# Kernel optimization log

Measured on AMD Instinct MI355X. Metric: run time of the kernel, lower is better.

Reference implementation:

```python
import jax, jax.numpy as jnp
import numpy as np
from jax import lax

B, C, D, H, W = 4, 384, 16, 16, 16
DSTATE, DCONV, EXPAND = 16, 4, 2
DIN = C * EXPAND            # 768
DTRANK = (C + 15) // 16     # 24
EPS = 1e-5


def setup_inputs() -> dict:
    ks = jax.random.split(jax.random.key(0), 12)
    g = lambda k, shape, s=0.02: jax.random.normal(k, shape, jnp.float32) * s
    return {
        "x": jax.random.normal(ks[0], (B, C, D, H, W), jnp.float32),
        "gsc_w1": g(ks[1], (C, C, 3, 3, 3)), "gsc_b1": jnp.zeros((C,), jnp.float32),
        "gsc_w2": g(ks[2], (C, C, 3, 3, 3)), "gsc_b2": jnp.zeros((C,), jnp.float32),
        "gsc_w3": g(ks[3], (C, C, 1, 1, 1)), "gsc_b3": jnp.zeros((C,), jnp.float32),
        "gsc_w4": g(ks[4], (C, C, 1, 1, 1)), "gsc_b4": jnp.zeros((C,), jnp.float32),
        "ln_g": jnp.ones((C,), jnp.float32), "ln_b": jnp.zeros((C,), jnp.float32),
        "in_proj_w": g(ks[5], (2 * DIN, C)),
        "conv1d_w": g(ks[6], (DIN, 1, DCONV), 0.1), "conv1d_b": jnp.zeros((DIN,), jnp.float32),
        "x_proj_w": g(ks[7], (DTRANK + 2 * DSTATE, DIN)),
        "dt_proj_w": g(ks[8], (DIN, DTRANK), 0.1), "dt_proj_b": jnp.full((DIN,), -4.0, jnp.float32),
        "A_log": jnp.log(jnp.tile(jnp.arange(1, DSTATE + 1, dtype=jnp.float32), (DIN, 1))),
        "D_skip": jnp.ones((DIN,), jnp.float32),
        "out_proj_w": g(ks[9], (C, DIN)),
    }


def _conv3d(x, w, b, pad):
    y = lax.conv_general_dilated(x, w, (1, 1, 1), [(pad, pad)] * 3,
                                 dimension_numbers=("NCDHW", "OIDHW", "NCDHW"))
    return y + b[None, :, None, None, None]


def _inorm(x):  # InstanceNorm3d, affine=False, biased variance
    m = x.mean((2, 3, 4), keepdims=True)
    v = x.var((2, 3, 4), keepdims=True)
    return (x - m) * lax.rsqrt(v + EPS)


def _forward(x, gsc_w1, gsc_b1, gsc_w2, gsc_b2, gsc_w3, gsc_b3, gsc_w4, gsc_b4,
             ln_g, ln_b, in_proj_w, conv1d_w, conv1d_b, x_proj_w,
             dt_proj_w, dt_proj_b, A_log, D_skip, out_proj_w):
    relu = jax.nn.relu
    # ---- GSC block (residual gated spatial conv) ----
    x1 = relu(_inorm(_conv3d(x, gsc_w1, gsc_b1, 1)))
    x1 = relu(_inorm(_conv3d(x1, gsc_w2, gsc_b2, 1)))
    x2 = relu(_inorm(_conv3d(x, gsc_w3, gsc_b3, 0)))
    xg = relu(_inorm(_conv3d(x1 + x2, gsc_w4, gsc_b4, 0))) + x
    # ---- MambaLayer: flatten voxels to tokens ----
    Bn = xg.shape[0]
    L = D * H * W
    t = xg.reshape(Bn, C, L).swapaxes(1, 2)                     # [B, L, C]
    mu = t.mean(-1, keepdims=True)
    var = t.var(-1, keepdims=True)
    tn = (t - mu) * lax.rsqrt(var + EPS) * ln_g + ln_b          # LayerNorm
    # ---- Mamba block ----
    xz = tn @ in_proj_w.T                                       # [B, L, 2*DIN]
    xin, z = jnp.split(xz, 2, axis=-1)
    xc = xin.swapaxes(1, 2)                                     # [B, DIN, L]
    xc = lax.conv_general_dilated(xc, conv1d_w, (1,), [(DCONV - 1, 0)],
                                  dimension_numbers=("NCH", "OIH", "NCH"),
                                  feature_group_count=DIN)      # causal depthwise conv
    u = jax.nn.silu(xc + conv1d_b[None, :, None]).swapaxes(1, 2)  # [B, L, DIN]
    dbl = u @ x_proj_w.T                                        # [B, L, DTRANK+2N]
    dt, Bm, Cm = jnp.split(dbl, [DTRANK, DTRANK + DSTATE], axis=-1)
    dt = jax.nn.softplus(dt @ dt_proj_w.T + dt_proj_b)          # [B, L, DIN]
    A = -jnp.exp(A_log)                                         # [DIN, N]

    def step(h, inp):  # h: [B, DIN, N]
        dt_t, B_t, C_t, u_t = inp
        dA = jnp.exp(dt_t[:, :, None] * A)
        h = dA * h + (dt_t * u_t)[:, :, None] * B_t[:, None, :]
        return h, jnp.einsum("bdn,bn->bd", h, C_t)

    h0 = jnp.zeros((Bn, DIN, DSTATE), x.dtype)
    _, ys = lax.scan(step, h0, (dt.swapaxes(0, 1), Bm.swapaxes(0, 1),
                                Cm.swapaxes(0, 1), u.swapaxes(0, 1)))
    y = ys.swapaxes(0, 1) + u * D_skip                          # [B, L, DIN]
    y = y * jax.nn.silu(z)
    out = y @ out_proj_w.T                                      # [B, L, C]
    return out.swapaxes(1, 2).reshape(Bn, C, D, H, W)


def reference(x, gsc_w1, gsc_b1, gsc_w2, gsc_b2, gsc_w3, gsc_b3, gsc_w4, gsc_b4,
              ln_g, ln_b, in_proj_w, conv1d_w, conv1d_b, x_proj_w,
              dt_proj_w, dt_proj_b, A_log, D_skip, out_proj_w):
    return _forward(x, gsc_w1, gsc_b1, gsc_w2, gsc_b2, gsc_w3, gsc_b3, gsc_w4, gsc_b4,
                    ln_g, ln_b, in_proj_w, conv1d_w, conv1d_b, x_proj_w,
                    dt_proj_w, dt_proj_b, A_log, D_skip, out_proj_w)
```

## Files before the change

### kernel.cpp

```cpp
#include <hip/hip_runtime.h>
#include <math.h>

#define CDIM 384
#define SDIM 4096
#define BDIM 4
#define DINC 768
#define NST  16
#define NCHUNK 64
#define LCHUNK 64
#define PSTRIDE 6291456

typedef unsigned short ushort_t;
typedef unsigned int uint_t;
typedef __attribute__((ext_vector_type(4))) float f32x4;
typedef __attribute__((ext_vector_type(8))) short bf16x8;

__device__ __forceinline__ ushort_t f2bf(float f) {
    union { float f; uint_t u; } v; v.f = f;
    uint_t r = v.u + 0x7FFFu + ((v.u >> 16) & 1u);
    return (ushort_t)(r >> 16);
}
__device__ __forceinline__ float bf2f(ushort_t u) {
    union { uint_t i; float f; } v; v.i = ((uint_t)u) << 16; return v.f;
}
__device__ __forceinline__ uint_t pk2(float a, float b) {
    return (uint_t)f2bf(a) | ((uint_t)f2bf(b) << 16);
}
__device__ __forceinline__ void gl16(const ushort_t* g, ushort_t* l) {
    __builtin_amdgcn_global_load_lds(
        (const __attribute__((address_space(1))) void*)(g),
        (__attribute__((address_space(3))) void*)(l), 16, 0, 0);
}

__device__ __forceinline__ void wconv_body(const float* __restrict__ W,
                                           ushort_t* __restrict__ Wb, int idx) {
    const float* wp = W + (size_t)idx * 27;
#pragma unroll
    for (int tap = 0; tap < 27; ++tap)
        Wb[(size_t)tap * (CDIM * CDIM) + idx] = f2bf(wp[tap]);
}
__device__ __forceinline__ void cvt_body(const float* __restrict__ src,
                                         ushort_t* __restrict__ dst, int i) {
    float4 v = ((const float4*)src)[i];
    uint2 o; o.x = pk2(v.x, v.y); o.y = pk2(v.z, v.w);
    ((uint2*)dst)[i] = o;
}
__global__ __launch_bounds__(256)
void prep_weights_kernel(const float* w1, const float* w2, const float* w3,
                         const float* w4, const float* ipw, const float* opw,
                         const float* xpw,
                         ushort_t* Wb1, ushort_t* Wb2, ushort_t* w3b, ushort_t* w4b,
                         ushort_t* ipwb, ushort_t* opwb, ushort_t* xpwb) {
    const int bid = blockIdx.x, t = threadIdx.x;
    if      (bid < 576)  wconv_body(w1, Wb1, bid * 256 + t);
    else if (bid < 1152) wconv_body(w2, Wb2, (bid - 576) * 256 + t);
    else if (bid < 1296) cvt_body(w3, w3b, (bid - 1152) * 256 + t);
    else if (bid < 1440) cvt_body(w4, w4b, (bid - 1296) * 256 + t);
    else if (bid < 2016) cvt_body(ipw, ipwb, (bid - 1440) * 256 + t);
    else if (bid < 2304) cvt_body(opw, opwb, (bid - 2016) * 256 + t);
    else                 cvt_body(xpw, xpwb, (bid - 2304) * 256 + t);
}

__global__ __launch_bounds__(384)
void pad_kernel(const float* __restrict__ src, ushort_t* __restrict__ Xp) {
    const int blk = blockIdx.x;
    const int b = blk >> 8, d = (blk >> 4) & 15, h = blk & 15;
    const int ci = threadIdx.x;
    const float* sp = src + (size_t)(b * CDIM + ci) * SDIM + d * 256 + h * 16;
    ushort_t* dp = Xp + ((((size_t)(b * 18 + d + 1) * 18) + (h + 1)) * 18 + 1) * CDIM + ci;
#pragma unroll
    for (int w = 0; w < 16; ++w)
        dp[(size_t)w * CDIM] = f2bf(sp[w]);
}

__global__ __launch_bounds__(384)
void pad_fuse2_kernel(const ushort_t* __restrict__ P0, const ushort_t* __restrict__ P1,
                      const float* __restrict__ stats, ushort_t* __restrict__ Xp) {
    const int blk = blockIdx.x;
    const int b = blk >> 8, d = (blk >> 4) & 15, h = blk & 15;
    const int ci = threadIdx.x;
    const size_t o = (size_t)(b * CDIM + ci) * SDIM + d * 256 + h * 16;
    const float m = stats[(b * CDIM + ci) * 2], r = stats[(b * CDIM + ci) * 2 + 1];
    union { uint4 q[2]; ushort_t u[16]; } a, c;
    a.q[0] = ((const uint4*)(P0 + o))[0]; a.q[1] = ((const uint4*)(P0 + o))[1];
    c.q[0] = ((const uint4*)(P1 + o))[0]; c.q[1] = ((const uint4*)(P1 + o))[1];
    ushort_t* dp = Xp + ((((size_t)(b * 18 + d + 1) * 18) + (h + 1)) * 18 + 1) * CDIM + ci;
#pragma unroll
    for (int w = 0; w < 16; ++w) {
        const float v = bf2f(a.u[w]) + bf2f(c.u[w]);
        dp[(size_t)w * CDIM] = f2bf(fmaxf((v - m) * r, 0.f));
    }
}

__global__ __launch_bounds__(384)
void pad_fuse3_kernel(const ushort_t* __restrict__ P0, const ushort_t* __restrict__ P1,
                      const float* __restrict__ st2, const ushort_t* __restrict__ C3,
                      const float* __restrict__ st3, ushort_t* __restrict__ Xp) {
    const int blk = blockIdx.x;
    const int b = blk >> 8, d = (blk >> 4) & 15, h = blk & 15;
    const int ci = threadIdx.x;
    const size_t o = (size_t)(b * CDIM + ci) * SDIM + d * 256 + h * 16;
    const float m2 = st2[(b * CDIM + ci) * 2], r2 = st2[(b * CDIM + ci) * 2 + 1];
    const float m3 = st3[(b * CDIM + ci) * 2], r3 = st3[(b * CDIM + ci) * 2 + 1];
    union { uint4 q[2]; ushort_t u[16]; } a, c, e;
    a.q[0] = ((const uint4*)(P0 + o))[0]; a.q[1] = ((const uint4*)(P0 + o))[1];
    c.q[0] = ((const uint4*)(P1 + o))[0]; c.q[1] = ((const uint4*)(P1 + o))[1];
    e.q[0] = ((const uint4*)(C3 + o))[0]; e.q[1] = ((const uint4*)(C3 + o))[1];
    ushort_t* dp = Xp + ((((size_t)(b * 18 + d + 1) * 18) + (h + 1)) * 18 + 1) * CDIM + ci;
#pragma unroll
    for (int w = 0; w < 16; ++w) {
        const float x1 = fmaxf((bf2f(a.u[w]) + bf2f(c.u[w]) - m2) * r2, 0.f);
        const float x2 = fmaxf((bf2f(e.u[w]) - m3) * r3, 0.f);
        dp[(size_t)w * CDIM] = f2bf(x1 + x2);
    }
}

template<int MODE>
__global__ __launch_bounds__(512)
void conv_kernel(const ushort_t* __restrict__ Xp, const ushort_t* __restrict__ Wb,
                 const ushort_t* __restrict__ W3, ushort_t* __restrict__ Y01,
                 ushort_t* __restrict__ Y2) {
    const int wid = blockIdx.x;
    const int ntid = wid & 63;
    const int rest = wid >> 6;
    const int co0 = (rest % 3) * 128;
    const int zz  = rest / 3;
    const int b  = ntid >> 4;
    const int d  = ntid & 15;
    const int t = threadIdx.x;
    const int lane = t & 63;
    const int wv = t >> 6;
    const int wy = wv >> 2, wx = wv & 3;

    const bool is1x1 = (MODE == 2) || (MODE == 1 && zz == 2);
    const ushort_t* Wsrc; int tap0, iters, kd0, kh0, kw0; ushort_t* Y;
    if (is1x1) {
        Wsrc = W3; tap0 = 0; iters = 12; kd0 = 1; kh0 = 1; kw0 = 1; Y = Y2;
    } else {
        Wsrc = Wb; tap0 = zz ? 14 : 0; iters = (zz ? 13 : 14) * 12;
        kd0 = zz ? 1 : 0; kh0 = zz ? 1 : 0; kw0 = zz ? 2 : 0;
        Y = Y01 + (size_t)zz * PSTRIDE;
    }

    __shared__ __align__(16) ushort_t As[4096];
    __shared__ __align__(16) ushort_t Bs[8192];

    f32x4 acc[4][4];
#pragma unroll
    for (int i = 0; i < 4; ++i)
#pragma unroll
        for (int j = 0; j < 4; ++j) acc[i][j] = (f32x4){0.f, 0.f, 0.f, 0.f};

    const int l4 = lane >> 2;
    const int cg = (((lane & 3) ^ ((lane >> 3) & 3)) << 3);
    const int rA = wv * 16 + l4;
    const int aTC = (co0 + rA) * CDIM + cg;
    int bTC[2];
#pragma unroll
    for (int i = 0; i < 2; ++i) {
        const int r = wv * 32 + i * 16 + l4;
        bTC[i] = ((r >> 4) * 18 + (r & 15)) * CDIM + cg;
    }
    ushort_t* lA = &As[wv * 512];
    ushort_t* lB[2] = { &Bs[wv * 1024], &Bs[wv * 1024 + 512] };

    int aoff = tap0 * (CDIM * CDIM);
    int goff = (((b * 18 + d + kd0) * 18 + kh0) * 18 + kw0) * CDIM;
    int c12 = 0, ckw = kw0, ckh = kh0;

    const int lm = lane & 15;
    const int sw8 = (((lane >> 4) ^ ((lm >> 1) & 3)) << 3);
    const int rA0 = (wy * 64 + lm) * 32 + sw8;
    const int rB0 = (wx * 64 + lm) * 32 + sw8;

    for (int idx = 0; idx < iters; ++idx) {
        gl16(Wsrc + aoff + aTC, lA);
        gl16(Xp + goff + bTC[0], lB[0]);
        gl16(Xp + goff + bTC[1], lB[1]);
        aoff += 32; goff += 32;
        if (++c12 == 12) {
            c12 = 0;
            aoff += CDIM * CDIM - CDIM;
            if (++ckw == 3) {
                ckw = 0;
                if (++ckh == 3) { ckh = 0; goff += 109440; }
                else goff += 5760;
            }
        }
        __syncthreads();
        bf16x8 af[4], bfr[4];
#pragma unroll
        for (int mi = 0; mi < 4; ++mi)
            af[mi] = *reinterpret_cast<const bf16x8*>(&As[rA0 + mi * 512]);
#pragma unroll
        for (int ni = 0; ni < 4; ++ni)
            bfr[ni] = *reinterpret_cast<const bf16x8*>(&Bs[rB0 + ni * 512]);
#pragma unroll
        for (int mi = 0; mi < 4; ++mi)
#pragma unroll
            for (int ni = 0; ni < 4; ++ni)
                acc[mi][ni] = __builtin_amdgcn_mfma_f32_16x16x32_bf16(
                    af[mi], bfr[ni], acc[mi][ni], 0, 0, 0);
        __syncthreads();
    }

    const int coB = co0 + wy * 64 + (lane >> 4) * 4;
#pragma unroll
    for (int mi = 0; mi < 4; ++mi) {
#pragma unroll
        for (int ni = 0; ni < 4; ++ni) {
            const int nl = wx * 64 + ni * 16 + lm;
            const int s = d * 256 + nl;
            ushort_t* yp = Y + ((size_t)b * CDIM + (coB + mi * 16)) * SDIM + s;
#pragma unroll
            for (int j = 0; j < 4; ++j)
                yp[(size_t)j * SDIM] = f2bf(acc[mi][ni][j]);
        }
    }
}

template<int EPI>
__global__ __launch_bounds__(256)
void gemm_gl_kernel(const ushort_t* __restrict__ A, const ushort_t* __restrict__ Bw,
                    void* __restrict__ Cv, void* __restrict__ C2v,
                    int M, int N, int K, int ldc, int nx) {
    const int wid = blockIdx.x;
    const int n0 = (wid % nx) * 128;
    const int m0 = (wid / nx) * 128;
    const int t = threadIdx.x;
    const int lane = t & 63;
    const int wv = t >> 6;
    const int wy = wv >> 1, wx = wv & 1;

    __shared__ __align__(16) ushort_t As[2][4096];
    __shared__ __align__(16) ushort_t Bs[2][4096];

    f32x4 acc[4][4];
#pragma unroll
    for (int i = 0; i < 4; ++i)
#pragma unroll
        for (int j = 0; j < 4; ++j) acc[i][j] = (f32x4){0.f, 0.f, 0.f, 0.f};

    const int l4 = lane >> 2;
    const int cg = (((lane & 3) ^ ((lane >> 3) & 3)) << 3);
    size_t aTC[2], bTC[2];
#pragma unroll
    for (int i = 0; i < 2; ++i) {
        const int r = wv * 32 + i * 16 + l4;
        aTC[i] = (size_t)(m0 + r) * K + cg;
        int br = n0 + r; if (br >= N) br = N - 1;
        bTC[i] = (size_t)br * K + cg;
    }

    const int lm = lane & 15;
    const int sw8 = (((lane >> 4) ^ ((lm >> 1) & 3)) << 3);
    const int rA0 = (wy * 64 + lm) * 32 + sw8;
    const int rB0 = (wx * 64 + lm) * 32 + sw8;

    auto stage = [&](int bf, int ko) {
        ushort_t* la = &As[bf][wv * 1024];
        ushort_t* lb = &Bs[bf][wv * 1024];
        gl16(A + aTC[0] + ko, la);
        gl16(A + aTC[1] + ko, la + 512);
        gl16(Bw + bTC[0] + ko, lb);
        gl16(Bw + bTC[1] + ko, lb + 512);
    };

    const int KI = K >> 5;
    stage(0, 0);
    __syncthreads();

    int buf = 0;
    for (int kk = 0; kk < KI; ++kk) {
        if (kk + 1 < KI) stage(buf ^ 1, (kk + 1) * 32);
        bf16x8 af[4], bfr[4];
#pragma unroll
        for (int mi = 0; mi < 4; ++mi)
            af[mi] = *reinterpret_cast<const bf16x8*>(&As[buf][rA0 + mi * 512]);
#pragma unroll
        for (int ni = 0; ni < 4; ++ni)
            bfr[ni] = *reinterpret_cast<const bf16x8*>(&Bs[buf][rB0 + ni * 512]);
#pragma unroll
        for (int mi = 0; mi < 4; ++mi)
#pragma unroll
            for (int ni = 0; ni < 4; ++ni)
                acc[mi][ni] = __builtin_amdgcn_mfma_f32_16x16x32_bf16(
                    af[mi], bfr[ni], acc[mi][ni], 0, 0, 0);
        __syncthreads();
        buf ^= 1;
    }

    const int mB = m0 + wy * 64 + (lane >> 4) * 4;
    const int nB = n0 + wx * 64 + lm;
#pragma unroll
    for (int mi = 0; mi < 4; ++mi) {
#pragma unroll
        for (int ni = 0; ni < 4; ++ni) {
            const int n = nB + ni * 16;
            if (EPI == 2) {
                const int mrow = mB + mi * 16;
                const int bb = mrow >> 12, l = mrow & 4095;
                float4 st = {acc[mi][ni][0], acc[mi][ni][1],
                             acc[mi][ni][2], acc[mi][ni][3]};
                *reinterpret_cast<float4*>(
                    (float*)Cv + ((size_t)(bb * CDIM + n)) * SDIM + l) = st;
            } else {
#pragma unroll
                for (int j = 0; j < 4; ++j) {
                    const int m = mB + mi * 16 + j;
                    const float v = acc[mi][ni][j];
                    if (EPI == 0) {
                        if (n < N) ((float*)Cv)[(size_t)m * ldc + n] = v;
                    } else {
                        if (n < DINC) ((ushort_t*)Cv)[(size_t)m * DINC + n] = f2bf(v);
                        else ((ushort_t*)C2v)[(size_t)m * DINC + (n - DINC)] = f2bf(v);
                    }
                }
            }
        }
    }
}

__device__ __forceinline__ void stats_reduce(float s, float ss, float* out) {
#pragma unroll
    for (int off = 32; off > 0; off >>= 1) {
        s += __shfl_down(s, off);
        ss += __shfl_down(ss, off);
    }
    __shared__ float rs[4], rss[4];
    const int wid = threadIdx.x >> 6;
    if ((threadIdx.x & 63) == 0) { rs[wid] = s; rss[wid] = ss; }
    __syncthreads();
    if (threadIdx.x == 0) {
        float S = rs[0] + rs[1] + rs[2] + rs[3];
        float SS = rss[0] + rss[1] + rss[2] + rss[3];
        float m = S * (1.f / SDIM);
        float var = SS * (1.f / SDIM) - m * m;
        out[0] = m;
        out[1] = rsqrtf(var + 1e-5f);
    }
}

__global__ __launch_bounds__(256)
void inorm_stats_combo_kernel(const ushort_t* __restrict__ P0,
                              const ushort_t* __restrict__ P1,
                              float* __restrict__ SA,
                              const ushort_t* __restrict__ X3,
                              float* __restrict__ SB) {
    const int bid = blockIdx.x;
    float s = 0.f, ss = 0.f;
    if (bid < 1536) {
        const ushort_t* p0 = P0 + (size_t)bid * SDIM;
        const ushort_t* p1 = P1 + (size_t)bid * SDIM;
        for (int i = threadIdx.x * 8; i < SDIM; i += 2048) {
            union { uint4 q; ushort_t u[8]; } a, c;
            a.q = *(const uint4*)(p0 + i);
            c.q = *(const uint4*)(p1 + i);
#pragma unroll
            for (int j = 0; j < 8; ++j) {
                const float v = bf2f(a.u[j]) + bf2f(c.u[j]);
                s += v; ss += v * v;
            }
        }
        stats_reduce(s, ss, SA + bid * 2);
    } else {
        const int bc = bid - 1536;
        const ushort_t* xp = X3 + (size_t)bc * SDIM;
        for (int i = threadIdx.x * 8; i < SDIM; i += 2048) {
            union { uint4 q; ushort_t u[8]; } a;
            a.q = *(const uint4*)(xp + i);
#pragma unroll
            for (int j = 0; j < 8; ++j) {
                const float v = bf2f(a.u[j]);
                s += v; ss += v * v;
            }
        }
        stats_reduce(s, ss, SB + bc * 2);
    }
}

__global__ __launch_bounds__(256)
void inorm_stats_kernel(const ushort_t* __restrict__ X, float* __restrict__ stats) {
    const int bc = blockIdx.x;
    const ushort_t* xp = X + (size_t)bc * SDIM;
    float s = 0.f, ss = 0.f;
    for (int i = threadIdx.x * 8; i < SDIM; i += 2048) {
        union { uint4 q; ushort_t u[8]; } a;
        a.q = *(const uint4*)(xp + i);
#pragma unroll
        for (int j = 0; j < 8; ++j) {
            const float v = bf2f(a.u[j]);
            s += v; ss += v * v;
        }
    }
    stats_reduce(s, ss, stats + bc * 2);
}

__global__ __launch_bounds__(256)
void layernorm_kernel(const ushort_t* __restrict__ C4, const float* __restrict__ stats,
                      const float* __restrict__ X, const float* __restrict__ gam,
                      const float* __restrict__ bet, ushort_t* __restrict__ Tn) {
    const int blk = blockIdx.x;
    const int b = blk >> 7;
    const int tile0 = (blk & 127) * 32;
    const int wv = threadIdx.x >> 6;
    const int lane = threadIdx.x & 63;
    const int l0 = tile0 + wv * 8;

    __shared__ ushort_t tile[32 * 384];

    float v[6][8];
    float s[8], ss[8];
#pragma unroll
    for (int t = 0; t < 8; ++t) { s[t] = 0.f; ss[t] = 0.f; }
    float g[6], be[6];

#pragma unroll
    for (int i = 0; i < 6; ++i) {
        const int c = lane + i * 64;
        g[i] = gam[c]; be[i] = bet[c];
        const size_t base = (size_t)(b * CDIM + c) * SDIM + l0;
        union { uint4 q; ushort_t u[8]; } cv;
        cv.q = *(const uint4*)(C4 + base);
        const float4 x0 = *(const float4*)(X + base);
        const float4 x1 = *(const float4*)(X + base + 4);
        const float xs[8] = {x0.x, x0.y, x0.z, x0.w, x1.x, x1.y, x1.z, x1.w};
        const float m = stats[(b * CDIM + c) * 2];
        const float r = stats[(b * CDIM + c) * 2 + 1];
#pragma unroll
        for (int t = 0; t < 8; ++t) {
            const float val = fmaxf((bf2f(cv.u[t]) - m) * r, 0.f) + xs[t];
            v[i][t] = val;
            s[t] += val; ss[t] += val * val;
        }
    }
#pragma unroll
    for (int off = 32; off > 0; off >>= 1) {
#pragma unroll
        for (int t = 0; t < 8; ++t) {
            s[t] += __shfl_xor(s[t], off);
            ss[t] += __shfl_xor(ss[t], off);
        }
    }
#pragma unroll
    for (int t = 0; t < 8; ++t) {
        const float mean = s[t] * (1.f / CDIM);
        const float rstd = rsqrtf(ss[t] * (1.f / CDIM) - mean * mean + 1e-5f);
        const int trow = (wv * 8 + t) * 384;
#pragma unroll
        for (int i = 0; i < 6; ++i) {
            const int c = lane + i * 64;
            tile[trow + c] = f2bf((v[i][t] - mean) * rstd * g[i] + be[i]);
        }
    }
    __syncthreads();
    uint4* dst = (uint4*)(Tn + ((size_t)b * 4096 + tile0) * CDIM);
    const uint4* srcp = (const uint4*)tile;
#pragma unroll
    for (int k = 0; k < 6; ++k)
        dst[k * 256 + threadIdx.x] = srcp[k * 256 + threadIdx.x];
}

__global__ __launch_bounds__(256)
void gemm_dtproj_kernel(const float* __restrict__ A, const float* __restrict__ B,
                        ushort_t* __restrict__ C, const float* __restrict__ bias,
                        int M, int N, int K, int lda, int ldb, int ldc) {
    __shared__ __align__(16) float As[16][132];
    __shared__ __align__(16) float Bs[16][68];
    const int t = threadIdx.x;
    const int m0 = blockIdx.y * 128;
    const int n0 = blockIdx.x * 64;

    float acc[8][4];
#pragma unroll
    for (int i = 0; i < 8; ++i)
#pragma unroll
        for (int j = 0; j < 4; ++j) acc[i][j] = 0.f;

    const int mr = (t & 15) * 8;
    const int nr = (t >> 4) * 4;

    for (int k0 = 0; k0 < K; k0 += 16) {
#pragma unroll
        for (int idx = 0; idx < 8; ++idx) {
            const int e = idx * 256 + t;
            const int k = e & 15, m = e >> 4;
            float v = 0.f;
            if (k0 + k < K) v = A[(size_t)(m0 + m) * lda + (k0 + k)];
            As[k][m] = v;
        }
#pragma unroll
        for (int idx = 0; idx < 4; ++idx) {
            const int e = idx * 256 + t;
            const int k = e & 15, n = e >> 4;
            float v = 0.f;
            if ((n0 + n) < N && (k0 + k) < K) v = B[(size_t)(n0 + n) * ldb + (k0 + k)];
            Bs[k][n] = v;
        }
        __syncthreads();
#pragma unroll
        for (int k = 0; k < 16; ++k) {
            float4 a0 = *(const float4*)&As[k][mr];
            float4 a1 = *(const float4*)&As[k][mr + 4];
            float4 b0 = *(const float4*)&Bs[k][nr];
            const float av[8] = {a0.x, a0.y, a0.z, a0.w, a1.x, a1.y, a1.z, a1.w};
            const float bv[4] = {b0.x, b0.y, b0.z, b0.w};
#pragma unroll
            for (int i = 0; i < 8; ++i)
#pragma unroll
                for (int j = 0; j < 4; ++j)
                    acc[i][j] = fmaf(av[i], bv[j], acc[i][j]);
        }
        __syncthreads();
    }

#pragma unroll
    for (int i = 0; i < 8; ++i) {
        const int m = m0 + mr + i;
#pragma unroll
        for (int j = 0; j < 4; ++j) {
            const int n = n0 + nr + j;
            if (n >= N) continue;
            float v = acc[i][j] + bias[n];
            v = (v > 20.f) ? v : log1pf(__expf(v));
            C[(size_t)m * ldc + n] = f2bf(v);
        }
    }
}

__global__ __launch_bounds__(256)
void dwconv_silu_kernel(const ushort_t* __restrict__ Xin, const float* __restrict__ W,
                        const float* __restrict__ bias, ushort_t* __restrict__ U) {
    const int dch = blockIdx.x * 256 + threadIdx.x;
    const int l0 = blockIdx.y * 4, b = blockIdx.z;
    const float4 w4 = ((const float4*)W)[dch];
    const float wk[4] = {w4.x, w4.y, w4.z, w4.w};
    const float bs = bias[dch];
    const size_t base = ((size_t)b * 4096 + l0) * DINC + dch;
    float r[7];
#pragma unroll
    for (int k = 0; k < 7; ++k) {
        const int ll = l0 - 3 + k;
        r[k] = (ll >= 0) ? bf2f(Xin[base + (size_t)(k - 3) * DINC]) : 0.f;
    }
#pragma unroll
    for (int j = 0; j < 4; ++j) {
        float acc = bs;
#pragma unroll
        for (int k = 0; k < 4; ++k) acc = fmaf(r[j + k], wk[k], acc);
        U[base + (size_t)j * DINC] = f2bf(acc / (1.f + __expf(-acc)));
    }
}

__global__ __launch_bounds__(256)
void scan_phase1_kernel(const ushort_t* __restrict__ DT, const ushort_t* __restrict__ U,
                        const float* __restrict__ DBL, const float* __restrict__ A_log,
                        float* __restrict__ HOUT, float* __restrict__ SDT) {
    const int b = blockIdx.z, chunk = blockIdx.y;
    const int dch = blockIdx.x * 256 + threadIdx.x;
    float Arow[16];
#pragma unroll
    for (int n = 0; n < NST; ++n) Arow[n] = -__expf(A_log[dch * NST + n]);

    __shared__ float bcs[LCHUNK][16];
    const size_t tokbase = (size_t)b * 4096 + chunk * LCHUNK;
#pragma unroll
    for (int idx = 0; idx < 4; ++idx) {
        const int e = idx * 256 + threadIdx.x;
        bcs[e >> 4][e & 15] = DBL[(tokbase + (e >> 4)) * 56 + 24 + (e & 15)];
    }
    __syncthreads();

    size_t off = tokbase * DINC + dch;
    float h[16];
#pragma unroll
    for (int n = 0; n < NST; ++n) h[n] = 0.f;
    float sdt = 0.f;
    float cdt = bf2f(DT[off]), cu = bf2f(U[off]);
    for (int t = 0; t < LCHUNK; ++t) {
        float ndt = 0.f, nu = 0.f;
        if (t < LCHUNK - 1) { ndt = bf2f(DT[off + DINC]); nu = bf2f(U[off + DINC]); }
        sdt += cdt;
        const float du = cdt * cu;
#pragma unroll
        for (int n = 0; n < NST; ++n)
            h[n] = __expf(cdt * Arow[n]) * h[n] + du * bcs[t][n];
        off += DINC;
        cdt = ndt; cu = nu;
    }
    float* hp = HOUT + (((size_t)(b * DINC + dch) * NCHUNK + chunk) << 4);
#pragma unroll
    for (int n = 0; n < NST; ++n) hp[n] = h[n];
    SDT[(size_t)(b * DINC + dch) * NCHUNK + chunk] = sdt;
}

__global__ __launch_bounds__(256)
void scan_phase2_kernel(float* __restrict__ HOUT, const float* __restrict__ SDT,
                        const float* __restrict__ A_log) {
    const int t = blockIdx.x * 256 + threadIdx.x;
    const int b = t / (DINC * NST);
    const int rem = t - b * (DINC * NST);
    const int d = rem >> 4, n = rem & 15;
    const float An = -__expf(A_log[d * NST + n]);
    float* hp = HOUT + (((size_t)(b * DINC + d) * NCHUNK) << 4) + n;
    const float* sp = SDT + (size_t)(b * DINC + d) * NCHUNK;
    float H = 0.f;
    for (int c = 0; c < NCHUNK; ++c) {
        const float tmp = hp[c * 16];
        const float dA = __expf(An * sp[c]);
        hp[c * 16] = H;
        H = dA * H + tmp;
    }
}

__global__ __launch_bounds__(256)
void scan_phase3_kernel(ushort_t* __restrict__ DT, const ushort_t* __restrict__ U,
                        const float* __restrict__ DBL, const ushort_t* __restrict__ Z,
                        const float* __restrict__ A_log, const float* __restrict__ D_skip,
                        const float* __restrict__ HOUT) {
    const int b = blockIdx.z, chunk = blockIdx.y;
    const int dch = blockIdx.x * 256 + threadIdx.x;
    float Arow[16];
#pragma unroll
    for (int n = 0; n < NST; ++n) Arow[n] = -__expf(A_log[dch * NST + n]);
    const float Dsk = D_skip[dch];

    __shared__ float bcs[LCHUNK][32];
    const size_t tokbase = (size_t)b * 4096 + chunk * LCHUNK;
#pragma unroll
    for (int idx = 0; idx < 8; ++idx) {
        const int e = idx * 256 + threadIdx.x;
        bcs[e >> 5][e & 31] = DBL[(tokbase + (e >> 5)) * 56 + 24 + (e & 31)];
    }
    __syncthreads();

    float h[16];
    const float* hp = HOUT + (((size_t)(b * DINC + dch) * NCHUNK + chunk) << 4);
#pragma unroll
    for (int n = 0; n < NST; ++n) h[n] = hp[n];

    size_t off = tokbase * DINC + dch;
    float cdt = bf2f(DT[off]), cu = bf2f(U[off]), cz = bf2f(Z[off]);
    for (int t = 0; t < LCHUNK; ++t) {
        float ndt = 0.f, nu = 0.f, nz = 0.f;
        if (t < LCHUNK - 1) {
            ndt = bf2f(DT[off + DINC]); nu = bf2f(U[off + DINC]); nz = bf2f(Z[off + DINC]);
        }
        const float du = cdt * cu;
        float y = 0.f;
#pragma unroll
        for (int n = 0; n < NST; ++n) {
            h[n] = __expf(cdt * Arow[n]) * h[n] + du * bcs[t][n];
            y = fmaf(h[n], bcs[t][16 + n], y);
        }
        y += cu * Dsk;
        const float sz = cz / (1.f + __expf(-cz));
        DT[off] = f2bf(y * sz);
        off += DINC;
        cdt = ndt; cu = nu; cz = nz;
    }
}

extern "C" void kernel_launch(void* const* d_in, const int* in_sizes, int n_in,
                              void* d_out, int out_size, void* d_ws, size_t ws_size,
                              hipStream_t stream) {
    (void)in_sizes; (void)n_in; (void)out_size; (void)ws_size;
    const float* x         = (const float*)d_in[0];
    const float* w1        = (const float*)d_in[1];
    const float* w2        = (const float*)d_in[3];
    const float* w3        = (const float*)d_in[5];
    const float* w4        = (const float*)d_in[7];
    const float* ln_g      = (const float*)d_in[9];
    const float* ln_b      = (const float*)d_in[10];
    const float* in_proj_w = (const float*)d_in[11];
    const float* conv1d_w  = (const float*)d_in[12];
    const float* conv1d_b  = (const float*)d_in[13];
    const float* x_proj_w  = (const float*)d_in[14];
    const float* dt_proj_w = (const float*)d_in[15];
    const float* dt_proj_b = (const float*)d_in[16];
    const float* A_log     = (const float*)d_in[17];
    const float* D_skip    = (const float*)d_in[18];
    const float* out_proj_w= (const float*)d_in[19];
    float* out = (float*)d_out;

    float* ws = (float*)d_ws;
    float* R0 = ws;
    float* R1 = ws + 6291456;
    float* R2 = ws + 12582912;
    float* R3 = ws + 25165824;
    float* R4 = ws + 37748736;

    ushort_t* P0    = (ushort_t*)R0;
    ushort_t* P1    = P0 + PSTRIDE;
    ushort_t* C34   = (ushort_t*)R3;
    ushort_t* Wb1   = (ushort_t*)R2;
    ushort_t* Xp    = (ushort_t*)(R2 + 2097152);
    ushort_t* w3b   = (ushort_t*)(R2 + 6576128);
    ushort_t* w4b   = (ushort_t*)(R2 + 6649856);
    ushort_t* Wb2   = (ushort_t*)(R2 + 6723584);
    float*    SA    = R4;
    float*    SB    = R4 + 4096;
    ushort_t* ipwb  = (ushort_t*)(R4 + 6291456);
    ushort_t* opwb  = (ushort_t*)(R4 + 6586368);
    ushort_t* xpwb  = (ushort_t*)(R4 + 6733824);
    ushort_t* tnb   = (ushort_t*)R0;
    float*    DBL   = R0 + 3145728;
    float*    HOUT  = R1;
    float*    SDT   = R1 + 3145728;
    ushort_t* XIN   = (ushort_t*)R2;
    ushort_t* Zb    = (ushort_t*)R3;
    ushort_t* Ub    = (ushort_t*)R4;
    ushort_t* DTb   = (ushort_t*)R2;

    const size_t XP_BYTES = (size_t)4 * 18 * 18 * 18 * CDIM * 2;

    hipMemsetAsync(Xp, 0, XP_BYTES, stream);
    prep_weights_kernel<<<2346, 256, 0, stream>>>(
        w1, w2, w3, w4, in_proj_w, out_proj_w, x_proj_w,
        Wb1, Wb2, w3b, w4b, ipwb, opwb, xpwb);
    pad_kernel<<<1024, 384, 0, stream>>>(x, Xp);
    conv_kernel<1><<<576, 512, 0, stream>>>(Xp, Wb1, w3b, P0, C34);
    inorm_stats_combo_kernel<<<3072, 256, 0, stream>>>(P0, P1, SA, C34, SB);
    pad_fuse2_kernel<<<1024, 384, 0, stream>>>(P0, P1, SA, Xp);
    conv_kernel<0><<<384, 512, 0, stream>>>(Xp, Wb2, nullptr, P0, nullptr);
    inorm_stats_combo_kernel<<<1536, 256, 0, stream>>>(P0, P1, SA, nullptr, nullptr);
    pad_fuse3_kernel<<<1024, 384, 0, stream>>>(P0, P1, SA, C34, SB, Xp);
    conv_kernel<2><<<192, 512, 0, stream>>>(Xp, nullptr, w4b, nullptr, C34);
    inorm_stats_kernel<<<1536, 256, 0, stream>>>(C34, SA);
    layernorm_kernel<<<512, 256, 0, stream>>>(C34, SA, x, ln_g, ln_b, tnb);
    gemm_gl_kernel<1><<<1536, 256, 0, stream>>>(
        tnb, ipwb, XIN, Zb, 16384, 1536, CDIM, 0, 12);
    dwconv_silu_kernel<<<dim3(3, 1024, 4), 256, 0, stream>>>(XIN, conv1d_w, conv1d_b, Ub);
    gemm_gl_kernel<0><<<128, 256, 0, stream>>>(
        Ub, xpwb, DBL, nullptr, 16384, 56, DINC, 56, 1);
    gemm_dtproj_kernel<<<dim3(12, 128), 256, 0, stream>>>(
        DBL, dt_proj_w, DTb, dt_proj_b, 16384, DINC, 24, 56, 24, DINC);
    scan_phase1_kernel<<<dim3(3, NCHUNK, 4), 256, 0, stream>>>(
        DTb, Ub, DBL, A_log, HOUT, SDT);
    scan_phase2_kernel<<<192, 256, 0, stream>>>(HOUT, SDT, A_log);
    scan_phase3_kernel<<<dim3(3, NCHUNK, 4), 256, 0, stream>>>(
        DTb, Ub, DBL, Zb, A_log, D_skip, HOUT);
    gemm_gl_kernel<2><<<384, 256, 0, stream>>>(
        DTb, opwb, out, nullptr, 16384, CDIM, DINC, 0, 3);
}
```

Measured before the change: 731.3 us.

## Split 3x3x3 conv reduction into four tap chunks for more parallel blocks

The 27-tap 3D convolutions are now split along the tap dimension into four partial sums (7,7,7,6 taps) instead of two, doubling the grid to 768 blocks. The 1x1 convolution moves into its own launch. The stats and pad kernels now sum four bf16 partial buffers. The aim is better CU occupancy and load balance on the conv GEMMs, at the cost of extra partial-sum memory traffic, more bf16 rounding of partials, and one extra launch.

```diff
diff --git a/kernel.cpp b/kernel.cpp
--- a/kernel.cpp
+++ b/kernel.cpp
@@ -74,42 +74,49 @@
 }
 
 __global__ __launch_bounds__(384)
-void pad_fuse2_kernel(const ushort_t* __restrict__ P0, const ushort_t* __restrict__ P1,
-                      const float* __restrict__ stats, ushort_t* __restrict__ Xp) {
+void pad_fuse2_kernel(const ushort_t* __restrict__ P, const float* __restrict__ stats,
+                      ushort_t* __restrict__ Xp) {
     const int blk = blockIdx.x;
     const int b = blk >> 8, d = (blk >> 4) & 15, h = blk & 15;
     const int ci = threadIdx.x;
     const size_t o = (size_t)(b * CDIM + ci) * SDIM + d * 256 + h * 16;
     const float m = stats[(b * CDIM + ci) * 2], r = stats[(b * CDIM + ci) * 2 + 1];
-    union { uint4 q[2]; ushort_t u[16]; } a, c;
-    a.q[0] = ((const uint4*)(P0 + o))[0]; a.q[1] = ((const uint4*)(P0 + o))[1];
-    c.q[0] = ((const uint4*)(P1 + o))[0]; c.q[1] = ((const uint4*)(P1 + o))[1];
+    union { uint4 q[2]; ushort_t u[16]; } p[4];
+#pragma unroll
+    for (int z = 0; z < 4; ++z) {
+        p[z].q[0] = ((const uint4*)(P + (size_t)z * PSTRIDE + o))[0];
+        p[z].q[1] = ((const uint4*)(P + (size_t)z * PSTRIDE + o))[1];
+    }
     ushort_t* dp = Xp + ((((size_t)(b * 18 + d + 1) * 18) + (h + 1)) * 18 + 1) * CDIM + ci;
 #pragma unroll
     for (int w = 0; w < 16; ++w) {
-        const float v = bf2f(a.u[w]) + bf2f(c.u[w]);
+        const float v = bf2f(p[0].u[w]) + bf2f(p[1].u[w]) + bf2f(p[2].u[w]) + bf2f(p[3].u[w]);
         dp[(size_t)w * CDIM] = f2bf(fmaxf((v - m) * r, 0.f));
     }
 }
 
 __global__ __launch_bounds__(384)
-void pad_fuse3_kernel(const ushort_t* __restrict__ P0, const ushort_t* __restrict__ P1,
-                      const float* __restrict__ st2, const ushort_t* __restrict__ C3,
-                      const float* __restrict__ st3, ushort_t* __restrict__ Xp) {
+void pad_fuse3_kernel(const ushort_t* __restrict__ P, const float* __restrict__ st2,
+                      const ushort_t* __restrict__ C3, const float* __restrict__ st3,
+                      ushort_t* __restrict__ Xp) {
     const int blk = blockIdx.x;
     const int b = blk >> 8, d = (blk >> 4) & 15, h = blk & 15;
     const int ci = threadIdx.x;
     const size_t o = (size_t)(b * CDIM + ci) * SDIM + d * 256 + h * 16;
     const float m2 = st2[(b * CDIM + ci) * 2], r2 = st2[(b * CDIM + ci) * 2 + 1];
     const float m3 = st3[(b * CDIM + ci) * 2], r3 = st3[(b * CDIM + ci) * 2 + 1];
-    union { uint4 q[2]; ushort_t u[16]; } a, c, e;
-    a.q[0] = ((const uint4*)(P0 + o))[0]; a.q[1] = ((const uint4*)(P0 + o))[1];
-    c.q[0] = ((const uint4*)(P1 + o))[0]; c.q[1] = ((const uint4*)(P1 + o))[1];
+    union { uint4 q[2]; ushort_t u[16]; } p[4], e;
+#pragma unroll
+    for (int z = 0; z < 4; ++z) {
+        p[z].q[0] = ((const uint4*)(P + (size_t)z * PSTRIDE + o))[0];
+        p[z].q[1] = ((const uint4*)(P + (size_t)z * PSTRIDE + o))[1];
+    }
     e.q[0] = ((const uint4*)(C3 + o))[0]; e.q[1] = ((const uint4*)(C3 + o))[1];
     ushort_t* dp = Xp + ((((size_t)(b * 18 + d + 1) * 18) + (h + 1)) * 18 + 1) * CDIM + ci;
 #pragma unroll
     for (int w = 0; w < 16; ++w) {
-        const float x1 = fmaxf((bf2f(a.u[w]) + bf2f(c.u[w]) - m2) * r2, 0.f);
+        const float sum = bf2f(p[0].u[w]) + bf2f(p[1].u[w]) + bf2f(p[2].u[w]) + bf2f(p[3].u[w]);
+        const float x1 = fmaxf((sum - m2) * r2, 0.f);
         const float x2 = fmaxf((bf2f(e.u[w]) - m3) * r3, 0.f);
         dp[(size_t)w * CDIM] = f2bf(x1 + x2);
     }
@@ -117,9 +124,8 @@
 
 template<int MODE>
 __global__ __launch_bounds__(512)
-void conv_kernel(const ushort_t* __restrict__ Xp, const ushort_t* __restrict__ Wb,
-                 const ushort_t* __restrict__ W3, ushort_t* __restrict__ Y01,
-                 ushort_t* __restrict__ Y2) {
+void conv_kernel(const ushort_t* __restrict__ Xp, const ushort_t* __restrict__ Wsrc,
+                 ushort_t* __restrict__ Ybase) {
     const int wid = blockIdx.x;
     const int ntid = wid & 63;
     const int rest = wid >> 6;
@@ -132,14 +138,14 @@
     const int wv = t >> 6;
     const int wy = wv >> 2, wx = wv & 3;
 
-    const bool is1x1 = (MODE == 2) || (MODE == 1 && zz == 2);
-    const ushort_t* Wsrc; int tap0, iters, kd0, kh0, kw0; ushort_t* Y;
-    if (is1x1) {
-        Wsrc = W3; tap0 = 0; iters = 12; kd0 = 1; kh0 = 1; kw0 = 1; Y = Y2;
+    int tap0, iters, kd0, kh0, kw0; ushort_t* Y;
+    if (MODE == 2) {
+        tap0 = 0; iters = 12; kd0 = 1; kh0 = 1; kw0 = 1; Y = Ybase;
     } else {
-        Wsrc = Wb; tap0 = zz ? 14 : 0; iters = (zz ? 13 : 14) * 12;
-        kd0 = zz ? 1 : 0; kh0 = zz ? 1 : 0; kw0 = zz ? 2 : 0;
-        Y = Y01 + (size_t)zz * PSTRIDE;
+        tap0 = 7 * zz; iters = (zz == 3 ? 6 : 7) * 12;
+        kd0 = tap0 / 9; const int r9 = tap0 - kd0 * 9;
+        kh0 = r9 / 3; kw0 = r9 - kh0 * 3;
+        Y = Ybase + (size_t)zz * PSTRIDE;
     }
 
     __shared__ __align__(16) ushort_t As[4096];
@@ -342,23 +348,21 @@
 }
 
 __global__ __launch_bounds__(256)
-void inorm_stats_combo_kernel(const ushort_t* __restrict__ P0,
-                              const ushort_t* __restrict__ P1,
-                              float* __restrict__ SA,
-                              const ushort_t* __restrict__ X3,
-                              float* __restrict__ SB) {
+void inorm_stats_combo_kernel(const ushort_t* __restrict__ P, float* __restrict__ SA,
+                              const ushort_t* __restrict__ X3, float* __restrict__ SB) {
     const int bid = blockIdx.x;
     float s = 0.f, ss = 0.f;
     if (bid < 1536) {
-        const ushort_t* p0 = P0 + (size_t)bid * SDIM;
-        const ushort_t* p1 = P1 + (size_t)bid * SDIM;
+        const size_t row = (size_t)bid * SDIM;
         for (int i = threadIdx.x * 8; i < SDIM; i += 2048) {
-            union { uint4 q; ushort_t u[8]; } a, c;
-            a.q = *(const uint4*)(p0 + i);
-            c.q = *(const uint4*)(p1 + i);
+            union { uint4 q; ushort_t u[8]; } p[4];
+#pragma unroll
+            for (int z = 0; z < 4; ++z)
+                p[z].q = *(const uint4*)(P + (size_t)z * PSTRIDE + row + i);
 #pragma unroll
             for (int j = 0; j < 8; ++j) {
-                const float v = bf2f(a.u[j]) + bf2f(c.u[j]);
+                const float v = bf2f(p[0].u[j]) + bf2f(p[1].u[j])
+                              + bf2f(p[2].u[j]) + bf2f(p[3].u[j]);
                 s += v; ss += v * v;
             }
         }
@@ -690,8 +694,7 @@
     float* R3 = ws + 25165824;
     float* R4 = ws + 37748736;
 
-    ushort_t* P0    = (ushort_t*)R0;
-    ushort_t* P1    = P0 + PSTRIDE;
+    ushort_t* P     = (ushort_t*)R0;
     ushort_t* C34   = (ushort_t*)R3;
     ushort_t* Wb1   = (ushort_t*)R2;
     ushort_t* Xp    = (ushort_t*)(R2 + 2097152);
@@ -719,13 +722,14 @@
         w1, w2, w3, w4, in_proj_w, out_proj_w, x_proj_w,
         Wb1, Wb2, w3b, w4b, ipwb, opwb, xpwb);
     pad_kernel<<<1024, 384, 0, stream>>>(x, Xp);
-    conv_kernel<1><<<576, 512, 0, stream>>>(Xp, Wb1, w3b, P0, C34);
-    inorm_stats_combo_kernel<<<3072, 256, 0, stream>>>(P0, P1, SA, C34, SB);
-    pad_fuse2_kernel<<<1024, 384, 0, stream>>>(P0, P1, SA, Xp);
-    conv_kernel<0><<<384, 512, 0, stream>>>(Xp, Wb2, nullptr, P0, nullptr);
-    inorm_stats_combo_kernel<<<1536, 256, 0, stream>>>(P0, P1, SA, nullptr, nullptr);
-    pad_fuse3_kernel<<<1024, 384, 0, stream>>>(P0, P1, SA, C34, SB, Xp);
-    conv_kernel<2><<<192, 512, 0, stream>>>(Xp, nullptr, w4b, nullptr, C34);
+    conv_kernel<0><<<768, 512, 0, stream>>>(Xp, Wb1, P);
+    conv_kernel<2><<<192, 512, 0, stream>>>(Xp, w3b, C34);
+    inorm_stats_combo_kernel<<<3072, 256, 0, stream>>>(P, SA, C34, SB);
+    pad_fuse2_kernel<<<1024, 384, 0, stream>>>(P, SA, Xp);
+    conv_kernel<0><<<768, 512, 0, stream>>>(Xp, Wb2, P);
+    inorm_stats_combo_kernel<<<1536, 256, 0, stream>>>(P, SA, nullptr, nullptr);
+    pad_fuse3_kernel<<<1024, 384, 0, stream>>>(P, SA, C34, SB, Xp);
+    conv_kernel<2><<<192, 512, 0, stream>>>(Xp, w4b, C34);
     inorm_stats_kernel<<<1536, 256, 0, stream>>>(C34, SA);
     layernorm_kernel<<<512, 256, 0, stream>>>(C34, SA, x, ln_g, ln_b, tnb);
     gemm_gl_kernel<1><<<1536, 256, 0, stream>>>(
```

New measurement: 826.8 us. 1.13x slower.

## Double-buffer LDS tiles in conv implicit-GEMM to overlap loads with MFMA

Applied to the files above, without the earlier changes.

Doubles the shared-memory A/B tiles and issues the global-to-LDS loads for the next K-step before computing on the current buffer. Explicit vmcnt waits and raw barriers replace the two full __syncthreads per iteration. The aim is to hide global load latency behind MFMA work in the 3x3x3 and 1x1 convolution GEMMs. LDS use doubles, which may reduce occupancy. Correctness depends on the hand-written waitcnt counts matching the three loads issued per stage.

```diff
diff --git a/kernel.cpp b/kernel.cpp
--- a/kernel.cpp
+++ b/kernel.cpp
@@ -142,8 +142,8 @@
         Y = Y01 + (size_t)zz * PSTRIDE;
     }
 
-    __shared__ __align__(16) ushort_t As[4096];
-    __shared__ __align__(16) ushort_t Bs[8192];
+    __shared__ __align__(16) ushort_t As[2][4096];
+    __shared__ __align__(16) ushort_t Bs[2][8192];
 
     f32x4 acc[4][4];
 #pragma unroll
@@ -161,8 +161,6 @@
         const int r = wv * 32 + i * 16 + l4;
         bTC[i] = ((r >> 4) * 18 + (r & 15)) * CDIM + cg;
     }
-    ushort_t* lA = &As[wv * 512];
-    ushort_t* lB[2] = { &Bs[wv * 1024], &Bs[wv * 1024 + 512] };
 
     int aoff = tap0 * (CDIM * CDIM);
     int goff = (((b * 18 + d + kd0) * 18 + kh0) * 18 + kw0) * CDIM;
@@ -173,10 +171,12 @@
     const int rA0 = (wy * 64 + lm) * 32 + sw8;
     const int rB0 = (wx * 64 + lm) * 32 + sw8;
 
-    for (int idx = 0; idx < iters; ++idx) {
-        gl16(Wsrc + aoff + aTC, lA);
-        gl16(Xp + goff + bTC[0], lB[0]);
-        gl16(Xp + goff + bTC[1], lB[1]);
+    auto stage = [&](int bf) {
+        ushort_t* la = &As[bf][wv * 512];
+        ushort_t* lb = &Bs[bf][wv * 1024];
+        gl16(Wsrc + aoff + aTC, la);
+        gl16(Xp + goff + bTC[0], lb);
+        gl16(Xp + goff + bTC[1], lb + 512);
         aoff += 32; goff += 32;
         if (++c12 == 12) {
             c12 = 0;
@@ -187,21 +187,38 @@
                 else goff += 5760;
             }
         }
-        __syncthreads();
+    };
+
+    stage(0);
+    asm volatile("s_waitcnt vmcnt(0)" ::: "memory");
+    __builtin_amdgcn_s_barrier();
+
+    int buf = 0;
+    for (int idx = 0; idx < iters; ++idx) {
+        const bool more = (idx + 1) < iters;
+        if (more) {
+            stage(buf ^ 1);
+            asm volatile("s_waitcnt vmcnt(3)" ::: "memory");
+        } else {
+            asm volatile("s_waitcnt vmcnt(0)" ::: "memory");
+        }
+        __builtin_amdgcn_s_barrier();
+        __builtin_amdgcn_sched_barrier(0);
         bf16x8 af[4], bfr[4];
 #pragma unroll
         for (int mi = 0; mi < 4; ++mi)
-            af[mi] = *reinterpret_cast<const bf16x8*>(&As[rA0 + mi * 512]);
+            af[mi] = *reinterpret_cast<const bf16x8*>(&As[buf][rA0 + mi * 512]);
 #pragma unroll
         for (int ni = 0; ni < 4; ++ni)
-            bfr[ni] = *reinterpret_cast<const bf16x8*>(&Bs[rB0 + ni * 512]);
+            bfr[ni] = *reinterpret_cast<const bf16x8*>(&Bs[buf][rB0 + ni * 512]);
 #pragma unroll
         for (int mi = 0; mi < 4; ++mi)
 #pragma unroll
             for (int ni = 0; ni < 4; ++ni)
                 acc[mi][ni] = __builtin_amdgcn_mfma_f32_16x16x32_bf16(
                     af[mi], bfr[ni], acc[mi][ni], 0, 0, 0);
-        __syncthreads();
+        __builtin_amdgcn_s_barrier();
+        buf ^= 1;
     }
 
     const int coB = co0 + wy * 64 + (lane >> 4) * 4;
```

Result: no change. 722.1 us (-1.3%).
